# Kernel optimization log

Measured on AMD Instinct MI355X. Metric: run time of the kernel, lower is better.

## Reference

```python
import jax, jax.numpy as jnp
import numpy as np

NUM_HEADS = 16


def setup_inputs() -> dict:
    key = jax.random.key(0)
    k1, k2, k3 = jax.random.split(key, 3)
    T, B, E = 2048, 2, 1024
    x = jax.random.normal(k1, (T, B, E), dtype=jnp.float32)
    in_proj_w = jax.random.normal(k2, (E, 3 * E), dtype=jnp.float32) * (E ** -0.5)
    in_proj_b = jnp.zeros((3 * E,), dtype=jnp.float32)
    out_w = jax.random.normal(k3, (E, E), dtype=jnp.float32) * (E ** -0.5)
    out_b = jnp.zeros((E,), dtype=jnp.float32)
    return {"x": x, "in_proj_w": in_proj_w, "in_proj_b": in_proj_b,
            "out_w": out_w, "out_b": out_b}


def reference(x, in_proj_w, in_proj_b, out_w, out_b):
    # x: (tgt_len, bsz, embed_dim) -- seq-first, self-attention (q is k is v)
    T, B, E = x.shape
    H = NUM_HEADS
    D = E // H
    scaling = D ** -0.5
    # packed in-projection: einsum('bne,ef->bnf') over (T,B,E)
    proj = jnp.einsum('tbe,ef->tbf', x, in_proj_w) + in_proj_b
    q, k, v = jnp.split(proj, 3, axis=-1)  # each (T, B, E)
    # reshape to (T, B*H, D) then transpose to (B*H, T, D)
    q = q.reshape(T, B * H, D).transpose(1, 0, 2)
    k = k.reshape(T, B * H, D).transpose(1, 0, 2)
    v = v.reshape(T, B * H, D).transpose(1, 0, 2)
    # full O(T^2) attention matrix, scaling applied after QK^T as in source
    attn = jnp.einsum('bie,bje->bij', q, k) * scaling  # (B*H, T, T)
    attn = jax.nn.softmax(attn, axis=-1)
    out = jnp.einsum('bij,bje->bie', attn, v)  # (B*H, T, D)
    # faithful to source: reshape directly (no head transpose-back)
    out = out.reshape(B, T, E)
    out = jnp.einsum('bte,ef->btf', out, out_w) + out_b
    return out
```

## Files before the change

### kernel.cpp

```cpp
#include <hip/hip_runtime.h>
#include <stdint.h>

#define TSEQ 2048
#define NB 2
#define EMB 1024
#define NHEAD 16
#define HDIM 64
#define KSPLIT 4
#define NT (TSEQ / KSPLIT / 64)
#define QSCALE 0.18033688f

typedef __bf16 bf16x8 __attribute__((ext_vector_type(8)));
typedef __bf16 bf16x4 __attribute__((ext_vector_type(4)));
typedef float f32x4 __attribute__((ext_vector_type(4)));

__device__ __forceinline__ void gload_lds16(const void* g, void* lds) {
    __builtin_amdgcn_global_load_lds(
        (const __attribute__((address_space(1))) unsigned int*)g,
        (__attribute__((address_space(3))) unsigned int*)lds, 16, 0, 0);
}

__global__ __launch_bounds__(256) void cvt_x_kernel(
    const float* __restrict__ x, __bf16* __restrict__ xb)
{
    const size_t idx = ((size_t)blockIdx.x * 256 + threadIdx.x) * 4;
    float4 v = *(const float4*)(x + idx);
    bf16x4 o = { (__bf16)v.x, (__bf16)v.y, (__bf16)v.z, (__bf16)v.w };
    *(bf16x4*)(xb + idx) = o;
}

__global__ __launch_bounds__(256) void transpose_cvt_kernel(
    const float* __restrict__ w_in, const float* __restrict__ w_out,
    __bf16* __restrict__ wiT, __bf16* __restrict__ whT)
{
    __shared__ float tile[32][33];
    int bx = blockIdx.x;
    const int by = blockIdx.y;
    const float* src; __bf16* dst; int sn;
    if (bx < 96) { src = w_in;  dst = wiT; sn = 3072; }
    else         { bx -= 96; src = w_out; dst = whT; sn = 1024; }
    const int tx = threadIdx.x, ty = threadIdx.y;
    #pragma unroll
    for (int i = 0; i < 4; ++i)
        tile[ty + i * 8][tx] = src[(size_t)(by * 32 + ty + i * 8) * sn + bx * 32 + tx];
    __syncthreads();
    #pragma unroll
    for (int i = 0; i < 4; ++i) {
        float v = tile[tx][ty + i * 8];
        dst[(size_t)(bx * 32 + ty + i * 8) * 1024 + by * 32 + tx] = (__bf16)v;
    }
}

__global__ __launch_bounds__(256) void gemm_qkv_kernel(
    const __bf16* __restrict__ A, const __bf16* __restrict__ BT,
    const float* __restrict__ bias,
    __bf16* __restrict__ Oq, __bf16* __restrict__ Ok, __bf16* __restrict__ Ov)
{
    __shared__ __align__(16) __bf16 As[128 * 64];
    __shared__ __align__(16) __bf16 Bs[128 * 64];
    const int tid = threadIdx.x;
    const int wave = tid >> 6, lane = tid & 63;
    const int l16 = lane & 15, quad = lane >> 4;
    const int wm = wave >> 1, wn = wave & 1;
    const int m0 = blockIdx.y * 128, n0 = blockIdx.x * 128;

    f32x4 acc[4][4];
    #pragma unroll
    for (int mt = 0; mt < 4; ++mt)
        #pragma unroll
        for (int nt = 0; nt < 4; ++nt)
            #pragma unroll
            for (int r = 0; r < 4; ++r) acc[mt][nt][r] = 0.f;

    int smrow[4], schunk[4], sbase[4];
    #pragma unroll
    for (int i = 0; i < 4; ++i) {
        int linear = (wave * 4 + i) * 64 + lane;
        smrow[i] = linear >> 3;
        schunk[i] = (linear & 7) ^ (smrow[i] & 7);
        sbase[i] = (wave * 4 + i) * 512;
    }

    for (int k0 = 0; k0 < 1024; k0 += 64) {
        #pragma unroll
        for (int i = 0; i < 4; ++i) {
            gload_lds16(A + (size_t)(m0 + smrow[i]) * 1024 + k0 + schunk[i] * 8,
                        As + sbase[i]);
            gload_lds16(BT + (size_t)(n0 + smrow[i]) * 1024 + k0 + schunk[i] * 8,
                        Bs + sbase[i]);
        }
        __syncthreads();
        #pragma unroll
        for (int kk = 0; kk < 2; ++kk) {
            bf16x8 am[4], bn[4];
            #pragma unroll
            for (int mt = 0; mt < 4; ++mt) {
                int row = wm * 64 + mt * 16 + l16;
                int c = (kk * 4 + quad) ^ (row & 7);
                am[mt] = *(const bf16x8*)(As + row * 64 + c * 8);
            }
            #pragma unroll
            for (int nt = 0; nt < 4; ++nt) {
                int row = wn * 64 + nt * 16 + l16;
                int c = (kk * 4 + quad) ^ (row & 7);
                bn[nt] = *(const bf16x8*)(Bs + row * 64 + c * 8);
            }
            #pragma unroll
            for (int mt = 0; mt < 4; ++mt)
                #pragma unroll
                for (int nt = 0; nt < 4; ++nt)
                    acc[mt][nt] = __builtin_amdgcn_mfma_f32_16x16x32_bf16(
                        am[mt], bn[nt], acc[mt][nt], 0, 0, 0);
        }
        __syncthreads();
    }

    #pragma unroll
    for (int nt = 0; nt < 4; ++nt) {
        const int col = n0 + wn * 64 + nt * 16 + l16;
        const float bv = bias[col];
        const int sec = col >> 10, f = col & 1023;
        const int h = f >> 6, d = f & 63;
        #pragma unroll
        for (int mt = 0; mt < 4; ++mt)
            #pragma unroll
            for (int r = 0; r < 4; ++r) {
                const int row = m0 + wm * 64 + mt * 16 + quad * 4 + r;
                float v = acc[mt][nt][r] + bv;
                const int t = row >> 1, b = row & 1;
                const int bh = b * NHEAD + h;
                const size_t idx = ((size_t)bh * TSEQ + t) * HDIM + d;
                if (sec == 0)
                    Oq[idx] = (__bf16)(v * QSCALE);
                else if (sec == 1)
                    Ok[idx] = (__bf16)v;
                else
                    Ov[idx] = (__bf16)v;
            }
    }
}

__global__ __launch_bounds__(256) void vtrans_kernel(
    const __bf16* __restrict__ V, __bf16* __restrict__ Vt)
{
    __shared__ __bf16 T[64 * 67];
    const int bh = blockIdx.y;
    const int t0 = blockIdx.x * 64;
    const int tid = threadIdx.x;
    const int r = tid >> 2;
    const int c = (tid & 3) * 16;
    const __bf16* src = V + ((size_t)bh * TSEQ + t0 + r) * HDIM + c;
    bf16x8 a = *(const bf16x8*)src;
    bf16x8 b = *(const bf16x8*)(src + 8);
    #pragma unroll
    for (int j = 0; j < 8; ++j) {
        T[r * 67 + c + j] = a[j];
        T[r * 67 + c + 8 + j] = b[j];
    }
    __syncthreads();
    const int dr = tid >> 2;
    const int tc = (tid & 3) * 16;
    bf16x8 o0, o1;
    #pragma unroll
    for (int j = 0; j < 8; ++j) {
        o0[j] = T[(tc + j) * 67 + dr];
        o1[j] = T[(tc + 8 + j) * 67 + dr];
    }
    __bf16* dst = Vt + ((size_t)bh * HDIM + dr) * TSEQ + t0 + tc;
    *(bf16x8*)dst = o0;
    *(bf16x8*)(dst + 8) = o1;
}

__global__ __launch_bounds__(256, 4) void attn_mfma_kernel(
    const __bf16* __restrict__ Q, const __bf16* __restrict__ K,
    const __bf16* __restrict__ Vt,
    __bf16* __restrict__ O0, __bf16* __restrict__ O1,
    __bf16* __restrict__ O2, __bf16* __restrict__ O3,
    float* __restrict__ L0, float* __restrict__ L1,
    float* __restrict__ L2, float* __restrict__ L3)
{
    __shared__ __align__(16) __bf16 Ks[64 * 64];
    __shared__ __align__(16) __bf16 Vs[2][64 * 64];
    __shared__ __align__(16) __bf16 Ps[4][16 * 64];

    const int tid  = threadIdx.x;
    const int wave = tid >> 6;
    const int lane = tid & 63;
    const int l16  = lane & 15;
    const int quad = lane >> 4;
    const int bh   = blockIdx.y;
    const int z    = blockIdx.z;
    const int q0   = blockIdx.x * 128 + wave * 32;
    const int kbase0 = z * (TSEQ / KSPLIT);

    __bf16* __restrict__ Opart = (z == 0) ? O0 : (z == 1) ? O1 : (z == 2) ? O2 : O3;
    float*  __restrict__ Lpart = (z == 0) ? L0 : (z == 1) ? L1 : (z == 2) ? L2 : L3;

    bf16x8 qf[2][2];
    #pragma unroll
    for (int mq = 0; mq < 2; ++mq) {
        const __bf16* Qrow = Q + ((size_t)bh * TSEQ + q0 + mq * 16 + l16) * HDIM;
        qf[mq][0] = *(const bf16x8*)(Qrow + quad * 8);
        qf[mq][1] = *(const bf16x8*)(Qrow + 32 + quad * 8);
    }

    f32x4 Oacc[2][4];
    #pragma unroll
    for (int mq = 0; mq < 2; ++mq)
        #pragma unroll
        for (int dt = 0; dt < 4; ++dt)
            #pragma unroll
            for (int r = 0; r < 4; ++r) Oacc[mq][dt][r] = 0.f;
    float l_part[2] = {0.f, 0.f};

    const __bf16* Kbase = K + ((size_t)bh * TSEQ + kbase0) * HDIM;
    const __bf16* Vbase = Vt + (size_t)bh * HDIM * TSEQ + kbase0;

    int srow[2], schk[2];
    #pragma unroll
    for (int i = 0; i < 2; ++i) {
        const int s = wave * 2 + i;
        srow[i] = s * 8 + (lane >> 3);
        schk[i] = (lane & 7) ^ (srow[i] & 7);
    }

#define STAGE(buf, kt)                                                        \
    {                                                                         \
        _Pragma("unroll")                                                     \
        for (int i = 0; i < 2; ++i) {                                         \
            const int s = wave * 2 + i;                                       \
            gload_lds16(Kbase + (size_t)((kt) * 64 + srow[i]) * HDIM          \
                            + schk[i] * 8,                                    \
                        Ks + s * 512);                                        \
            gload_lds16(Vbase + (size_t)srow[i] * TSEQ + (kt) * 64            \
                            + schk[i] * 8,                                    \
                        &Vs[buf][s * 512]);                                   \
        }                                                                     \
    }

    STAGE(0, 0);

    for (int kt = 0; kt < NT; ++kt) {
        const int buf = kt & 1;
        __syncthreads();

        bf16x8 kf[4][2];
        #pragma unroll
        for (int nt = 0; nt < 4; ++nt) {
            const int row = nt * 16 + l16;
            #pragma unroll
            for (int ch = 0; ch < 2; ++ch) {
                const int c = (quad + 4 * ch) ^ (row & 7);
                kf[nt][ch] = *(const bf16x8*)(&Ks[row * 64 + c * 8]);
            }
        }
        __syncthreads();
        if (kt + 1 < NT) STAGE(buf ^ 1, kt + 1);

        bf16x8 pa[2][2];
        #pragma unroll
        for (int mq = 0; mq < 2; ++mq) {
            #pragma unroll
            for (int nt = 0; nt < 4; ++nt) {
                f32x4 s = {0.f, 0.f, 0.f, 0.f};
                s = __builtin_amdgcn_mfma_f32_16x16x32_bf16(kf[nt][0], qf[mq][0], s, 0, 0, 0);
                s = __builtin_amdgcn_mfma_f32_16x16x32_bf16(kf[nt][1], qf[mq][1], s, 0, 0, 0);
                float p0 = exp2f(s[0]), p1 = exp2f(s[1]);
                float p2 = exp2f(s[2]), p3 = exp2f(s[3]);
                l_part[mq] += (p0 + p1) + (p2 + p3);
                bf16x4 pk = { (__bf16)p0, (__bf16)p1, (__bf16)p2, (__bf16)p3 };
                const int kidx = nt * 16 + quad * 4;
                const int pos = ((kidx >> 3) ^ (l16 & 7)) * 8 + (kidx & 7);
                *(bf16x4*)(&Ps[wave][l16 * 64 + pos]) = pk;
            }
            #pragma unroll
            for (int h = 0; h < 2; ++h) {
                const int c = (quad + 4 * h) ^ (l16 & 7);
                pa[mq][h] = *(const bf16x8*)(&Ps[wave][l16 * 64 + c * 8]);
            }
        }

        #pragma unroll
        for (int dt = 0; dt < 4; ++dt) {
            const int row = dt * 16 + l16;
            const int c0 = quad ^ (row & 7);
            const int c1 = (quad + 4) ^ (row & 7);
            bf16x8 v0 = *(const bf16x8*)(&Vs[buf][row * 64 + c0 * 8]);
            bf16x8 v1 = *(const bf16x8*)(&Vs[buf][row * 64 + c1 * 8]);
            #pragma unroll
            for (int mq = 0; mq < 2; ++mq) {
                Oacc[mq][dt] = __builtin_amdgcn_mfma_f32_16x16x32_bf16(
                    pa[mq][0], v0, Oacc[mq][dt], 0, 0, 0);
                Oacc[mq][dt] = __builtin_amdgcn_mfma_f32_16x16x32_bf16(
                    pa[mq][1], v1, Oacc[mq][dt], 0, 0, 0);
            }
        }
    }
#undef STAGE

    #pragma unroll
    for (int mq = 0; mq < 2; ++mq) {
        float v = l_part[mq];
        v += __shfl_xor(v, 16);
        v += __shfl_xor(v, 32);
        if (quad == 0)
            Lpart[(size_t)bh * TSEQ + q0 + mq * 16 + l16] = v;
    }

    const size_t base = ((size_t)bh * TSEQ + q0) * HDIM;
    #pragma unroll
    for (int mq = 0; mq < 2; ++mq)
        #pragma unroll
        for (int dt = 0; dt < 4; ++dt)
            #pragma unroll
            for (int r = 0; r < 4; ++r) {
                const size_t idx = base +
                    (size_t)(mq * 16 + quad * 4 + r) * HDIM + dt * 16 + l16;
                Opart[idx] = (__bf16)Oacc[mq][dt][r];
            }
}

__global__ __launch_bounds__(256) void normalize_kernel(
    const __bf16* __restrict__ O0, const __bf16* __restrict__ O1,
    const __bf16* __restrict__ O2, const __bf16* __restrict__ O3,
    const float* __restrict__ L0, const float* __restrict__ L1,
    const float* __restrict__ L2, const float* __restrict__ L3,
    __bf16* __restrict__ Ob)
{
    const size_t gid = (size_t)blockIdx.x * 256 + threadIdx.x;
    const size_t idx = gid * 8;
    const size_t qi = idx >> 6;
    const float inv = 1.f / (L0[qi] + L1[qi] + L2[qi] + L3[qi]);
    bf16x8 a = *(const bf16x8*)(O0 + idx);
    bf16x8 b = *(const bf16x8*)(O1 + idx);
    bf16x8 c = *(const bf16x8*)(O2 + idx);
    bf16x8 d = *(const bf16x8*)(O3 + idx);
    bf16x8 o;
    #pragma unroll
    for (int j = 0; j < 8; ++j)
        o[j] = (__bf16)((((float)a[j] + (float)b[j]) +
                         ((float)c[j] + (float)d[j])) * inv);
    *(bf16x8*)(Ob + idx) = o;
}

__global__ __launch_bounds__(256) void gemm_out_kernel(
    const __bf16* __restrict__ A, const __bf16* __restrict__ BT,
    const float* __restrict__ bias, float* __restrict__ out)
{
    __shared__ __align__(16) __bf16 As[64 * 64];
    __shared__ __align__(16) __bf16 Bs[64 * 64];
    const int tid = threadIdx.x;
    const int wave = tid >> 6, lane = tid & 63;
    const int l16 = lane & 15, quad = lane >> 4;
    const int wm = wave >> 1, wn = wave & 1;
    const int m0 = blockIdx.y * 64, n0 = blockIdx.x * 64;

    f32x4 acc[2][2];
    #pragma unroll
    for (int mt = 0; mt < 2; ++mt)
        #pragma unroll
        for (int nt = 0; nt < 2; ++nt)
            #pragma unroll
            for (int r = 0; r < 4; ++r) acc[mt][nt][r] = 0.f;

    int srow[2], schk[2], sbase[2];
    #pragma unroll
    for (int i = 0; i < 2; ++i) {
        const int s = wave * 2 + i;
        srow[i] = s * 8 + (lane >> 3);
        schk[i] = (lane & 7) ^ (srow[i] & 7);
        sbase[i] = s * 512;
    }

    for (int k0 = 0; k0 < 1024; k0 += 64) {
        #pragma unroll
        for (int i = 0; i < 2; ++i) {
            gload_lds16(A + (size_t)(m0 + srow[i]) * 1024 + k0 + schk[i] * 8,
                        As + sbase[i]);
            gload_lds16(BT + (size_t)(n0 + srow[i]) * 1024 + k0 + schk[i] * 8,
                        Bs + sbase[i]);
        }
        __syncthreads();
        #pragma unroll
        for (int kk = 0; kk < 2; ++kk) {
            bf16x8 am[2], bn[2];
            #pragma unroll
            for (int mt = 0; mt < 2; ++mt) {
                int row = wm * 32 + mt * 16 + l16;
                int c = (kk * 4 + quad) ^ (row & 7);
                am[mt] = *(const bf16x8*)(As + row * 64 + c * 8);
            }
            #pragma unroll
            for (int nt = 0; nt < 2; ++nt) {
                int row = wn * 32 + nt * 16 + l16;
                int c = (kk * 4 + quad) ^ (row & 7);
                bn[nt] = *(const bf16x8*)(Bs + row * 64 + c * 8);
            }
            #pragma unroll
            for (int mt = 0; mt < 2; ++mt)
                #pragma unroll
                for (int nt = 0; nt < 2; ++nt)
                    acc[mt][nt] = __builtin_amdgcn_mfma_f32_16x16x32_bf16(
                        am[mt], bn[nt], acc[mt][nt], 0, 0, 0);
        }
        __syncthreads();
    }

    #pragma unroll
    for (int nt = 0; nt < 2; ++nt) {
        const int col = n0 + wn * 32 + nt * 16 + l16;
        const float bv = bias[col];
        #pragma unroll
        for (int mt = 0; mt < 2; ++mt)
            #pragma unroll
            for (int r = 0; r < 4; ++r) {
                const int row = m0 + wm * 32 + mt * 16 + quad * 4 + r;
                out[(size_t)row * 1024 + col] = acc[mt][nt][r] + bv;
            }
    }
}

extern "C" void kernel_launch(void* const* d_in, const int* in_sizes, int n_in,
                              void* d_out, int out_size, void* d_ws, size_t ws_size,
                              hipStream_t stream) {
    const float* x     = (const float*)d_in[0];
    const float* w_in  = (const float*)d_in[1];
    const float* b_in  = (const float*)d_in[2];
    const float* w_out = (const float*)d_in[3];
    const float* b_out = (const float*)d_in[4];
    float* out = (float*)d_out;

    const size_t M1 = (size_t)1024 * 1024;
    __bf16* ws  = (__bf16*)d_ws;
    __bf16* xb  = ws;
    __bf16* wiT = xb  + 4 * M1;
    __bf16* whT = wiT + 3 * M1;
    __bf16* Qb  = whT + 1 * M1;
    __bf16* Kb  = Qb  + 4 * M1;
    __bf16* Vt  = Kb  + 4 * M1;
    __bf16* O0  = Vt  + 4 * M1;
    __bf16* O1  = O0  + 4 * M1;
    float*  L0  = (float*)(O1 + 4 * M1);
    float*  L1  = L0 + 65536;
    float*  L2  = L1 + 65536;
    float*  L3  = L2 + 65536;
    __bf16* Vb  = (__bf16*)d_out;
    __bf16* O2  = (__bf16*)d_out;
    __bf16* O3  = O2 + 4 * M1;
    __bf16* Ob  = xb;

    cvt_x_kernel<<<4096, 256, 0, stream>>>(x, xb);
    transpose_cvt_kernel<<<dim3(128, 32), dim3(32, 8), 0, stream>>>(
        w_in, w_out, wiT, whT);
    gemm_qkv_kernel<<<dim3(24, 32), 256, 0, stream>>>(
        xb, wiT, b_in, Qb, Kb, Vb);
    vtrans_kernel<<<dim3(32, 32), 256, 0, stream>>>(Vb, Vt);
    attn_mfma_kernel<<<dim3(16, 32, KSPLIT), 256, 0, stream>>>(
        Qb, Kb, Vt, O0, O1, O2, O3, L0, L1, L2, L3);
    normalize_kernel<<<2048, 256, 0, stream>>>(
        O0, O1, O2, O3, L0, L1, L2, L3, Ob);
    gemm_out_kernel<<<dim3(16, 64), 256, 0, stream>>>(
        Ob, whT, b_out, out);
}
```

Baseline: 205.3 us.

## Switch attention to 32x32x16 MFMA with register-resident P via permlane swap

Rewrites the attention inner loop to use 32x32x16 bf16 MFMAs. The softmax probabilities are packed with v_cvt_pk_bf16 and rearranged across lanes with v_permlane32_swap, so they stay in registers instead of going through an LDS round trip. K is now double-buffered like V, which removes the second barrier per tile, and exp2 uses the hardware builtin. This cuts LDS traffic and synchronisation in the hot loop, at the cost of doubling K's LDS footprint and relying on the exact lane layout of the permlane swap being correct.

```diff
diff --git a/kernel.cpp b/kernel.cpp
--- a/kernel.cpp
+++ b/kernel.cpp
@@ -13,11 +13,37 @@
 typedef __bf16 bf16x8 __attribute__((ext_vector_type(8)));
 typedef __bf16 bf16x4 __attribute__((ext_vector_type(4)));
 typedef float f32x4 __attribute__((ext_vector_type(4)));
+typedef float f32x16 __attribute__((ext_vector_type(16)));
+typedef unsigned int u32x4 __attribute__((ext_vector_type(4)));
 
 __device__ __forceinline__ void gload_lds16(const void* g, void* lds) {
     __builtin_amdgcn_global_load_lds(
         (const __attribute__((address_space(1))) unsigned int*)g,
         (__attribute__((address_space(3))) unsigned int*)lds, 16, 0, 0);
+}
+
+__device__ __forceinline__ float fast_exp2(float x) {
+#if __has_builtin(__builtin_amdgcn_exp2f)
+    return __builtin_amdgcn_exp2f(x);
+#else
+    return exp2f(x);
+#endif
+}
+
+__device__ __forceinline__ unsigned cvt_pk_bf16(float lo, float hi) {
+    unsigned r;
+    asm("v_cvt_pk_bf16_f32 %0, %1, %2" : "=v"(r) : "v"(lo), "v"(hi));
+    return r;
+}
+
+__device__ __forceinline__ void swap32(unsigned& a, unsigned& b) {
+    asm("v_permlane32_swap_b32 %0, %1" : "+v"(a), "+v"(b));
+}
+
+__device__ __forceinline__ bf16x8 as_bf16x8(u32x4 u) {
+    union { u32x4 u; bf16x8 h; } c;
+    c.u = u;
+    return c.h;
 }
 
 __global__ __launch_bounds__(256) void cvt_x_kernel(
@@ -179,15 +205,15 @@
     float* __restrict__ L0, float* __restrict__ L1,
     float* __restrict__ L2, float* __restrict__ L3)
 {
-    __shared__ __align__(16) __bf16 Ks[64 * 64];
+    __shared__ __align__(16) __bf16 Ks[2][64 * 64];
     __shared__ __align__(16) __bf16 Vs[2][64 * 64];
-    __shared__ __align__(16) __bf16 Ps[4][16 * 64];
 
     const int tid  = threadIdx.x;
     const int wave = tid >> 6;
     const int lane = tid & 63;
-    const int l16  = lane & 15;
-    const int quad = lane >> 4;
+    const int l31  = lane & 31;
+    const int hi   = lane >> 5;
+    const int m7   = l31 & 7;
     const int bh   = blockIdx.y;
     const int z    = blockIdx.z;
     const int q0   = blockIdx.x * 128 + wave * 32;
@@ -196,22 +222,20 @@
     __bf16* __restrict__ Opart = (z == 0) ? O0 : (z == 1) ? O1 : (z == 2) ? O2 : O3;
     float*  __restrict__ Lpart = (z == 0) ? L0 : (z == 1) ? L1 : (z == 2) ? L2 : L3;
 
-    bf16x8 qf[2][2];
-    #pragma unroll
-    for (int mq = 0; mq < 2; ++mq) {
-        const __bf16* Qrow = Q + ((size_t)bh * TSEQ + q0 + mq * 16 + l16) * HDIM;
-        qf[mq][0] = *(const bf16x8*)(Qrow + quad * 8);
-        qf[mq][1] = *(const bf16x8*)(Qrow + 32 + quad * 8);
-    }
-
-    f32x4 Oacc[2][4];
-    #pragma unroll
-    for (int mq = 0; mq < 2; ++mq)
-        #pragma unroll
-        for (int dt = 0; dt < 4; ++dt)
-            #pragma unroll
-            for (int r = 0; r < 4; ++r) Oacc[mq][dt][r] = 0.f;
-    float l_part[2] = {0.f, 0.f};
+    bf16x8 qf[4];
+    {
+        const __bf16* Qrow = Q + ((size_t)bh * TSEQ + q0 + l31) * HDIM + 8 * hi;
+        #pragma unroll
+        for (int c = 0; c < 4; ++c)
+            qf[c] = *(const bf16x8*)(Qrow + 16 * c);
+    }
+
+    f32x16 Oacc[2];
+    #pragma unroll
+    for (int dt = 0; dt < 2; ++dt)
+        #pragma unroll
+        for (int r = 0; r < 16; ++r) Oacc[dt][r] = 0.f;
+    float l4[4] = {0.f, 0.f, 0.f, 0.f};
 
     const __bf16* Kbase = K + ((size_t)bh * TSEQ + kbase0) * HDIM;
     const __bf16* Vbase = Vt + (size_t)bh * HDIM * TSEQ + kbase0;
@@ -231,7 +255,7 @@
             const int s = wave * 2 + i;                                       \
             gload_lds16(Kbase + (size_t)((kt) * 64 + srow[i]) * HDIM          \
                             + schk[i] * 8,                                    \
-                        Ks + s * 512);                                        \
+                        &Ks[buf][s * 512]);                                   \
             gload_lds16(Vbase + (size_t)srow[i] * TSEQ + (kt) * 64            \
                             + schk[i] * 8,                                    \
                         &Vs[buf][s * 512]);                                   \
@@ -241,83 +265,69 @@
     STAGE(0, 0);
 
     for (int kt = 0; kt < NT; ++kt) {
-        const int buf = kt & 1;
+        const int b = kt & 1;
         __syncthreads();
-
-        bf16x8 kf[4][2];
-        #pragma unroll
-        for (int nt = 0; nt < 4; ++nt) {
-            const int row = nt * 16 + l16;
-            #pragma unroll
-            for (int ch = 0; ch < 2; ++ch) {
-                const int c = (quad + 4 * ch) ^ (row & 7);
-                kf[nt][ch] = *(const bf16x8*)(&Ks[row * 64 + c * 8]);
-            }
-        }
-        __syncthreads();
-        if (kt + 1 < NT) STAGE(buf ^ 1, kt + 1);
-
-        bf16x8 pa[2][2];
-        #pragma unroll
-        for (int mq = 0; mq < 2; ++mq) {
-            #pragma unroll
-            for (int nt = 0; nt < 4; ++nt) {
-                f32x4 s = {0.f, 0.f, 0.f, 0.f};
-                s = __builtin_amdgcn_mfma_f32_16x16x32_bf16(kf[nt][0], qf[mq][0], s, 0, 0, 0);
-                s = __builtin_amdgcn_mfma_f32_16x16x32_bf16(kf[nt][1], qf[mq][1], s, 0, 0, 0);
-                float p0 = exp2f(s[0]), p1 = exp2f(s[1]);
-                float p2 = exp2f(s[2]), p3 = exp2f(s[3]);
-                l_part[mq] += (p0 + p1) + (p2 + p3);
-                bf16x4 pk = { (__bf16)p0, (__bf16)p1, (__bf16)p2, (__bf16)p3 };
-                const int kidx = nt * 16 + quad * 4;
-                const int pos = ((kidx >> 3) ^ (l16 & 7)) * 8 + (kidx & 7);
-                *(bf16x4*)(&Ps[wave][l16 * 64 + pos]) = pk;
-            }
-            #pragma unroll
-            for (int h = 0; h < 2; ++h) {
-                const int c = (quad + 4 * h) ^ (l16 & 7);
-                pa[mq][h] = *(const bf16x8*)(&Ps[wave][l16 * 64 + c * 8]);
-            }
-        }
-
-        #pragma unroll
-        for (int dt = 0; dt < 4; ++dt) {
-            const int row = dt * 16 + l16;
-            const int c0 = quad ^ (row & 7);
-            const int c1 = (quad + 4) ^ (row & 7);
-            bf16x8 v0 = *(const bf16x8*)(&Vs[buf][row * 64 + c0 * 8]);
-            bf16x8 v1 = *(const bf16x8*)(&Vs[buf][row * 64 + c1 * 8]);
-            #pragma unroll
-            for (int mq = 0; mq < 2; ++mq) {
-                Oacc[mq][dt] = __builtin_amdgcn_mfma_f32_16x16x32_bf16(
-                    pa[mq][0], v0, Oacc[mq][dt], 0, 0, 0);
-                Oacc[mq][dt] = __builtin_amdgcn_mfma_f32_16x16x32_bf16(
-                    pa[mq][1], v1, Oacc[mq][dt], 0, 0, 0);
-            }
-        }
+        if (kt + 1 < NT) STAGE(b ^ 1, kt + 1);
+
+        u32x4 pa[4];
+        #pragma unroll
+        for (int s = 0; s < 2; ++s) {
+            f32x16 sacc;
+            #pragma unroll
+            for (int r = 0; r < 16; ++r) sacc[r] = 0.f;
+            #pragma unroll
+            for (int c = 0; c < 4; ++c) {
+                bf16x8 kf = *(const bf16x8*)(
+                    &Ks[b][(32 * s + l31) * 64 + (((c << 1) | hi) ^ m7) * 8]);
+                sacc = __builtin_amdgcn_mfma_f32_32x32x16_bf16(
+                    kf, qf[c], sacc, 0, 0, 0);
+            }
+            float p[16];
+            #pragma unroll
+            for (int r = 0; r < 16; ++r) {
+                p[r] = fast_exp2(sacc[r]);
+                l4[r & 3] += p[r];
+            }
+            unsigned x[8];
+            #pragma unroll
+            for (int i = 0; i < 8; ++i)
+                x[i] = cvt_pk_bf16(p[2 * i], p[2 * i + 1]);
+            swap32(x[0], x[2]); swap32(x[1], x[3]);
+            swap32(x[4], x[6]); swap32(x[5], x[7]);
+            pa[2 * s][0] = x[0]; pa[2 * s][1] = x[1];
+            pa[2 * s][2] = x[2]; pa[2 * s][3] = x[3];
+            pa[2 * s + 1][0] = x[4]; pa[2 * s + 1][1] = x[5];
+            pa[2 * s + 1][2] = x[6]; pa[2 * s + 1][3] = x[7];
+        }
+
+        #pragma unroll
+        for (int dt = 0; dt < 2; ++dt)
+            #pragma unroll
+            for (int ks = 0; ks < 4; ++ks) {
+                bf16x8 vf = *(const bf16x8*)(
+                    &Vs[b][(dt * 32 + l31) * 64 + (((ks << 1) | hi) ^ m7) * 8]);
+                Oacc[dt] = __builtin_amdgcn_mfma_f32_32x32x16_bf16(
+                    as_bf16x8(pa[ks]), vf, Oacc[dt], 0, 0, 0);
+            }
     }
 #undef STAGE
 
-    #pragma unroll
-    for (int mq = 0; mq < 2; ++mq) {
-        float v = l_part[mq];
-        v += __shfl_xor(v, 16);
+    {
+        float v = (l4[0] + l4[1]) + (l4[2] + l4[3]);
         v += __shfl_xor(v, 32);
-        if (quad == 0)
-            Lpart[(size_t)bh * TSEQ + q0 + mq * 16 + l16] = v;
+        if (hi == 0)
+            Lpart[(size_t)bh * TSEQ + q0 + l31] = v;
     }
 
     const size_t base = ((size_t)bh * TSEQ + q0) * HDIM;
     #pragma unroll
-    for (int mq = 0; mq < 2; ++mq)
-        #pragma unroll
-        for (int dt = 0; dt < 4; ++dt)
-            #pragma unroll
-            for (int r = 0; r < 4; ++r) {
-                const size_t idx = base +
-                    (size_t)(mq * 16 + quad * 4 + r) * HDIM + dt * 16 + l16;
-                Opart[idx] = (__bf16)Oacc[mq][dt][r];
-            }
+    for (int dt = 0; dt < 2; ++dt)
+        #pragma unroll
+        for (int r = 0; r < 16; ++r) {
+            const int q = (r & 3) + 8 * (r >> 2) + 4 * hi;
+            Opart[base + (size_t)q * HDIM + dt * 32 + l31] =
+                (__bf16)Oacc[dt][r];
+        }
 }
 
 __global__ __launch_bounds__(256) void normalize_kernel(
```

Measured after the change: 201.5 us. Within noise of the previous version (-1.9%).
